# Optimization experiments

Measured on AMD Instinct MI355X. Metric: run time of the kernel, lower is better.

## Reference

```python
import jax, jax.numpy as jnp
import numpy as np

N = 100000   # num nodes
E = 1200000  # num edges (before self-loops)
K = 2        # SGConv propagation hops


def _gcn_norm(edge_index, edge_weight):
    # PyG gcn_norm: add self-loops (weight 1) then symmetric normalization
    loop = jnp.arange(N, dtype=edge_index.dtype)
    src = jnp.concatenate([edge_index[0], loop])
    dst = jnp.concatenate([edge_index[1], loop])
    w = jnp.concatenate([edge_weight, jnp.ones((N,), edge_weight.dtype)])
    deg = jax.ops.segment_sum(w, dst, num_segments=N)
    dinv = jnp.where(deg > 0, jax.lax.rsqrt(deg), jnp.zeros_like(deg))
    norm = dinv[src] * w * dinv[dst]
    return src, dst, norm


def _sgconv(x, src, dst, norm, W, b):
    # K hops of A_hat @ x, then linear: x @ W.T + b
    for _ in range(K):
        x = jax.ops.segment_sum(norm[:, None] * x[src], dst, num_segments=N)
    return x @ W.T + b


def setup_inputs() -> dict:
    key = jax.random.key(0)
    k = jax.random.split(key, 6)
    d_in, d_hid, d_out = 64, 64, 40
    x = jax.random.normal(k[0], (N, d_in), jnp.float32)
    edge_index = jax.random.randint(k[1], (2, E), 0, N, jnp.int32)
    edge_weight = jnp.ones((E,), jnp.float32)
    W1 = jax.random.normal(k[2], (d_hid, d_in), jnp.float32) / np.sqrt(d_in)
    b1 = jnp.zeros((d_hid,), jnp.float32)
    W2 = jax.random.normal(k[3], (d_out, d_hid), jnp.float32) / np.sqrt(d_hid)
    b2 = jnp.zeros((d_out,), jnp.float32)
    return {"x": x, "edge_index": edge_index, "edge_weight": edge_weight,
            "W1": W1, "b1": b1, "W2": W2, "b2": b2}


def reference(x, edge_index, edge_weight, W1, b1, W2, b2):
    # eval mode: F.dropout(p=0.6, training=False) is identity
    src, dst, norm = _gcn_norm(edge_index, edge_weight)
    h = jax.nn.relu(_sgconv(x, src, dst, norm, W1, b1))
    out = _sgconv(h, src, dst, norm, W2, b2)
    return out
```

## Files before the change

kernel.cpp:

```cpp
#include <hip/hip_runtime.h>
#include <hip/hip_fp16.h>


#define SCAN_TPB 256
#define SCAN_ITEMS 8
#define SCAN_CHUNK (SCAN_TPB * SCAN_ITEMS)
#define P1_EDGES 2048
#define MAX_NB 784


__global__ __launch_bounds__(SCAN_TPB) void scan_partial_kernel(const int* __restrict__ cnt,
                                                                int* __restrict__ bsums, int N_) {
    int t = threadIdx.x;
    int base = blockIdx.x * SCAN_CHUNK + t * SCAN_ITEMS;
    int s = 0;
    #pragma unroll
    for (int j = 0; j < SCAN_ITEMS; ++j) { int i = base + j; if (i < N_) s += cnt[i]; }
    __shared__ int sm[SCAN_TPB];
    sm[t] = s; __syncthreads();
    for (int o = SCAN_TPB / 2; o > 0; o >>= 1) {
        if (t < o) sm[t] += sm[t + o];
        __syncthreads();
    }
    if (t == 0) bsums[blockIdx.x] = sm[0];
}

__global__ __launch_bounds__(1024) void scan_bsums_kernel(int* bsums, int nb,
                                                          int* out, int N_) {
    __shared__ int sm[1024];
    int t = threadIdx.x;
    int v = (t < nb) ? bsums[t] : 0;
    sm[t] = v; __syncthreads();
    for (int o = 1; o < 1024; o <<= 1) {
        int u = (t >= o) ? sm[t - o] : 0;
        __syncthreads();
        sm[t] += u;
        __syncthreads();
    }
    if (t < nb) bsums[t] = sm[t] - v;
    if (t == 1023) out[N_] = sm[1023];
}

__global__ __launch_bounds__(SCAN_TPB) void scan_final_kernel(const int* __restrict__ cnt,
                                                              const int* __restrict__ bsums,
                                                              int* __restrict__ out, int N_) {
    int t = threadIdx.x;
    int base = blockIdx.x * SCAN_CHUNK + t * SCAN_ITEMS;
    int loc[SCAN_ITEMS];
    int s = 0;
    #pragma unroll
    for (int j = 0; j < SCAN_ITEMS; ++j) {
        int i = base + j;
        int c = (i < N_) ? cnt[i] : 0;
        loc[j] = s; s += c;
    }
    __shared__ int sm[SCAN_TPB];
    sm[t] = s; __syncthreads();
    for (int o = 1; o < SCAN_TPB; o <<= 1) {
        int u = (t >= o) ? sm[t - o] : 0;
        __syncthreads();
        sm[t] += u;
        __syncthreads();
    }
    int excl = bsums[blockIdx.x] + sm[t] - s;
    #pragma unroll
    for (int j = 0; j < SCAN_ITEMS; ++j) {
        int i = base + j;
        if (i < N_) out[i] = excl + loc[j];
    }
}

__global__ __launch_bounds__(256) void p1_count_kernel(const int* __restrict__ ei,
                                                       int* __restrict__ coarseCnt,
                                                       int E_, int PB, int NB) {
    __shared__ int hist[MAX_NB];
    int tid = threadIdx.x;
    for (int u = tid; u < NB; u += 256) hist[u] = 0;
    __syncthreads();
    int base = blockIdx.x * P1_EDGES;
    #pragma unroll
    for (int j = 0; j < P1_EDGES / 512; ++j) {
        int e = base + j * 512 + tid * 2;
        if (e + 1 < E_) {
            int2 d2 = *(const int2*)&ei[E_ + e];
            atomicAdd(&hist[d2.x >> 7], 1);
            atomicAdd(&hist[d2.y >> 7], 1);
        } else if (e < E_) {
            atomicAdd(&hist[ei[E_ + e] >> 7], 1);
        }
    }
    __syncthreads();
    for (int u = tid; u < NB; u += 256) coarseCnt[u * PB + blockIdx.x] = hist[u];
}

__global__ __launch_bounds__(256) void p1_scatter_kernel(const int* __restrict__ ei,
                                                         const float* __restrict__ w,
                                                         const int* __restrict__ coarseOff,
                                                         int2* __restrict__ sorted,
                                                         int E_, int PB, int NB) {
    __shared__ int lcur[MAX_NB];
    int tid = threadIdx.x;
    for (int u = tid; u < NB; u += 256) lcur[u] = coarseOff[u * PB + blockIdx.x];
    __syncthreads();
    int base = blockIdx.x * P1_EDGES;
    #pragma unroll
    for (int j = 0; j < P1_EDGES / 512; ++j) {
        int e = base + j * 512 + tid * 2;
        if (e + 1 < E_) {
            int2   s2 = *(const int2*)&ei[e];
            int2   d2 = *(const int2*)&ei[E_ + e];
            float2 w2 = *(const float2*)&w[e];
            int p0 = atomicAdd(&lcur[d2.x >> 7], 1);
            sorted[p0] = make_int2(s2.x | ((d2.x & 127) << 17), __float_as_int(w2.x));
            int p1 = atomicAdd(&lcur[d2.y >> 7], 1);
            sorted[p1] = make_int2(s2.y | ((d2.y & 127) << 17), __float_as_int(w2.y));
        } else if (e < E_) {
            int dst = ei[E_ + e];
            int pos = atomicAdd(&lcur[dst >> 7], 1);
            sorted[pos] = make_int2(ei[e] | ((dst & 127) << 17), __float_as_int(w[e]));
        }
    }
}

__global__ __launch_bounds__(256) void p2_fine_kernel(const int2* __restrict__ sorted,
                                                      const int* __restrict__ coarseOff,
                                                      int2* __restrict__ edge,
                                                      int* __restrict__ row_ptr,
                                                      float* __restrict__ dinv,
                                                      int N_, int E_, int PB, int NB) {
    __shared__ int fcnt[128], fexc[128], fcur[128];
    __shared__ float fdeg[128];
    const int b = blockIdx.x;
    const int tid = threadIdx.x;
    const int start = coarseOff[b * PB];
    const int end = (b + 1 < NB) ? coarseOff[(b + 1) * PB] : E_;
    if (tid < 128) { fcnt[tid] = 0; fdeg[tid] = 1.0f; }
    __syncthreads();
    for (int p = start + tid; p < end; p += 256)
        atomicAdd(&fcnt[sorted[p].x >> 17], 1);
    __syncthreads();
    if (tid < 128) fexc[tid] = fcnt[tid];
    __syncthreads();
    for (int o = 1; o < 128; o <<= 1) {
        int v = (tid < 128 && tid >= o) ? fexc[tid - o] : 0;
        __syncthreads();
        if (tid < 128) fexc[tid] += v;
        __syncthreads();
    }
    const int node0 = b << 7;
    if (tid < 128) {
        fexc[tid] -= fcnt[tid];
        fcur[tid] = 0;
        int node = node0 + tid;
        if (node < N_) row_ptr[node] = start + fexc[tid];
    }
    __syncthreads();
    for (int p = start + tid; p < end; p += 256) {
        int2 pk = sorted[p];
        int fine = pk.x >> 17;
        int src  = pk.x & 0x1FFFF;
        int r = atomicAdd(&fcur[fine], 1);
        atomicAdd(&fdeg[fine], __int_as_float(pk.y));
        edge[start + fexc[fine] + r] = make_int2(src, pk.y);
    }
    __syncthreads();
    if (tid < 128) {
        int node = node0 + tid;
        if (node < N_) {
            float s = fdeg[tid];
            dinv[node] = (s > 0.f) ? (1.0f / sqrtf(s)) : 0.f;
        }
    }
    if (b == 0 && tid == 0) row_ptr[N_] = E_;
}

#define FMA_MIX_LO(accv, hbits, vw) \
    asm("v_fma_mix_f32 %0, %1, %2, %0 op_sel_hi:[1,0,0]" : "+v"(accv) : "v"(hbits), "v"(vw))
#define FMA_MIX_HI(accv, hbits, vw) \
    asm("v_fma_mix_f32 %0, %1, %2, %0 op_sel:[1,0,0] op_sel_hi:[1,0,0]" : "+v"(accv) : "v"(hbits), "v"(vw))

template<int NL, int EPI>
__global__ __launch_bounds__(256) void hop_h_kernel(const __half* __restrict__ xin,
                                                    void* __restrict__ xout,
                                                    const float* __restrict__ dinv,
                                                    const int* __restrict__ row_ptr,
                                                    const int2* __restrict__ edge,
                                                    const float* __restrict__ bias, int N_) {
    int wave = (blockIdx.x * blockDim.x + threadIdx.x) >> 6;
    int lane = threadIdx.x & 63;
    const int g   = lane >> 4;
    const int hl  = lane & 15;
    const int hle = (NL == 16) ? hl : min(hl, NL - 1);

    int nd = wave * 4 + g;
    bool real = nd < N_;
    int d = real ? nd : (N_ - 1);

    int e0 = row_ptr[d];
    int nE = real ? (row_ptr[d + 1] - e0) : 0;
    float di = dinv[d];
    float2 selfv = ((const float2*)(xin + (size_t)d * 64))[hle];
    float acc[4] = {0.f, 0.f, 0.f, 0.f};

    int maxNE = nE;
    maxNE = max(maxNE, __shfl_xor(maxNE, 16));
    maxNE = max(maxNE, __shfl_xor(maxNE, 32));

    for (int eb = 0; eb < maxNE; eb += 16) {
        int rem = nE - eb;
        int2 ev = (hl < rem) ? edge[e0 + eb + hl] : make_int2(d, 0);
        int mm = min(16, maxNE - eb);
        for (int j = 0; j < mm; j += 2) {
            int   s0 = __shfl(ev.x, (g << 4) | j);
            int   s1 = __shfl(ev.x, (g << 4) | (j + 1));
            float v0 = __shfl(__int_as_float(ev.y), (g << 4) | j);
            float v1 = __shfl(__int_as_float(ev.y), (g << 4) | (j + 1));
            float2 x0 = ((const float2*)(xin + (size_t)s0 * 64))[hle];
            float2 x1 = ((const float2*)(xin + (size_t)s1 * 64))[hle];
            FMA_MIX_LO(acc[0], x0.x, v0); FMA_MIX_HI(acc[1], x0.x, v0);
            FMA_MIX_LO(acc[2], x0.y, v0); FMA_MIX_HI(acc[3], x0.y, v0);
            FMA_MIX_LO(acc[0], x1.x, v1); FMA_MIX_HI(acc[1], x1.x, v1);
            FMA_MIX_LO(acc[2], x1.y, v1); FMA_MIX_HI(acc[3], x1.y, v1);
        }
    }
    const float one = 1.0f;
    FMA_MIX_LO(acc[0], selfv.x, one); FMA_MIX_HI(acc[1], selfv.x, one);
    FMA_MIX_LO(acc[2], selfv.y, one); FMA_MIX_HI(acc[3], selfv.y, one);

    float sc = (EPI == 0) ? di * di : di;
    #pragma unroll
    for (int u = 0; u < 4; ++u) acc[u] *= sc;

    if (real && hl < NL) {
        if constexpr (EPI == 0) {
            float2 pk;
            ((__half2*)&pk)[0] = __floats2half2_rn(acc[0], acc[1]);
            ((__half2*)&pk)[1] = __floats2half2_rn(acc[2], acc[3]);
            ((float2*)((__half*)xout + (size_t)d * 64))[hl] = pk;
        } else if constexpr (EPI == 1) {
            float4 bv = ((const float4*)bias)[hl];
            float2 pk;
            ((__half2*)&pk)[0] = __floats2half2_rn(fmaxf(acc[0] + bv.x, 0.f),
                                                   fmaxf(acc[1] + bv.y, 0.f));
            ((__half2*)&pk)[1] = __floats2half2_rn(fmaxf(acc[2] + bv.z, 0.f),
                                                   fmaxf(acc[3] + bv.w, 0.f));
            ((float2*)((__half*)xout + (size_t)d * 64))[hl] = pk;
        } else {
            float4 bv = ((const float4*)bias)[hl];
            float4 r = make_float4(acc[0] + bv.x, acc[1] + bv.y,
                                   acc[2] + bv.z, acc[3] + bv.w);
            *(float4*)((float*)xout + (size_t)d * 40 + hl * 4) = r;
        }
    }
}

template<int F, bool INH>
__global__ __launch_bounds__(256, 4) void linear_tiled_kernel(const void* __restrict__ hin,
                                                              __half* __restrict__ outp,
                                                              const float* __restrict__ W,
                                                              const float* __restrict__ dinv,
                                                              int N_) {
    constexpr int BM = 64;
    __shared__ float hs[BM * 64];
    __shared__ float ws[64 * 64];
    const int tid  = threadIdx.x;
    const int base = blockIdx.x * BM;

    for (int u = tid; u < 64 * 16; u += 256) {
        int f = u >> 4, kc = u & 15;
        float4 v = (f < F) ? ((const float4*)W)[f * 16 + kc]
                           : make_float4(0.f, 0.f, 0.f, 0.f);
        *(float4*)&ws[f * 64 + ((kc ^ ((f >> 2) & 7)) << 2)] = v;
    }
    const int lim = min(BM, N_ - base);
    for (int u = tid; u < BM * 16; u += 256) {
        int n = u >> 4, kc = u & 15;
        float4 v;
        if (n < lim) {
            if constexpr (INH) {
                float2 hv = ((const float2*)((const __half*)hin + (size_t)(base + n) * 64))[kc];
                const __half2* hh = (const __half2*)&hv;
                float2 a = __half22float2(hh[0]);
                float2 b = __half22float2(hh[1]);
                v = make_float4(a.x, a.y, b.x, b.y);
            } else {
                v = ((const float4*)((const float*)hin + (size_t)(base + n) * 64))[kc];
            }
        } else v = make_float4(0.f, 0.f, 0.f, 0.f);
        *(float4*)&hs[n * 64 + ((kc ^ ((n >> 2) & 7)) << 2)] = v;
    }
    __syncthreads();

    const int f0 = (tid & 15) << 2;
    const int n0 = (tid >> 4) << 2;
    float4 acc[4];
    #pragma unroll
    for (int i = 0; i < 4; ++i) acc[i] = make_float4(0.f, 0.f, 0.f, 0.f);

    #pragma unroll 2
    for (int kc = 0; kc < 16; ++kc) {
        float4 hv[4], wv[4];
        #pragma unroll
        for (int i = 0; i < 4; ++i) {
            int n = n0 + i;
            hv[i] = *(const float4*)&hs[n * 64 + ((kc ^ ((n >> 2) & 7)) << 2)];
        }
        #pragma unroll
        for (int j = 0; j < 4; ++j) {
            int f = f0 + j;
            wv[j] = *(const float4*)&ws[f * 64 + ((kc ^ ((f >> 2) & 7)) << 2)];
        }
        #pragma unroll
        for (int i = 0; i < 4; ++i) {
            acc[i].x = fmaf(hv[i].x, wv[0].x, acc[i].x);
            acc[i].x = fmaf(hv[i].y, wv[0].y, acc[i].x);
            acc[i].x = fmaf(hv[i].z, wv[0].z, acc[i].x);
            acc[i].x = fmaf(hv[i].w, wv[0].w, acc[i].x);
            acc[i].y = fmaf(hv[i].x, wv[1].x, acc[i].y);
            acc[i].y = fmaf(hv[i].y, wv[1].y, acc[i].y);
            acc[i].y = fmaf(hv[i].z, wv[1].z, acc[i].y);
            acc[i].y = fmaf(hv[i].w, wv[1].w, acc[i].y);
            acc[i].z = fmaf(hv[i].x, wv[2].x, acc[i].z);
            acc[i].z = fmaf(hv[i].y, wv[2].y, acc[i].z);
            acc[i].z = fmaf(hv[i].z, wv[2].z, acc[i].z);
            acc[i].z = fmaf(hv[i].w, wv[2].w, acc[i].z);
            acc[i].w = fmaf(hv[i].x, wv[3].x, acc[i].w);
            acc[i].w = fmaf(hv[i].y, wv[3].y, acc[i].w);
            acc[i].w = fmaf(hv[i].z, wv[3].z, acc[i].w);
            acc[i].w = fmaf(hv[i].w, wv[3].w, acc[i].w);
        }
    }

    if (f0 < F) {
        #pragma unroll
        for (int i = 0; i < 4; ++i) {
            int n = base + n0 + i;
            if (n < N_) {
                float dn = dinv[n];
                __half* o = outp + (size_t)n * 64 + f0;
                ((__half2*)o)[0] = __floats2half2_rn(acc[i].x * dn, acc[i].y * dn);
                ((__half2*)o)[1] = __floats2half2_rn(acc[i].z * dn, acc[i].w * dn);
            }
        }
    }
}

extern "C" void kernel_launch(void* const* d_in, const int* in_sizes, int n_in,
                              void* d_out, int out_size, void* d_ws, size_t ws_size,
                              hipStream_t stream) {
    const float* x   = (const float*)d_in[0];
    const int*   ei  = (const int*)d_in[1];
    const float* w   = (const float*)d_in[2];
    const float* W1  = (const float*)d_in[3];
    const float* b1  = (const float*)d_in[4];
    const float* W2  = (const float*)d_in[5];
    const float* b2  = (const float*)d_in[6];
    float* out = (float*)d_out;

    const int N_ = in_sizes[0] / 64;
    const int E_ = in_sizes[2];
    const int PB = (E_ + P1_EDGES - 1) / P1_EDGES;
    const int NB = (N_ + 127) >> 7;
    const int M  = NB * PB;

    char* ws = (char*)d_ws;
    size_t off = 0;
    auto alloc = [&](size_t bytes) { size_t o = off; off += (bytes + 255) & ~(size_t)255; return o; };
    float* dinv      = (float*)(ws + alloc((size_t)N_ * 4));
    int*   row_ptr   = (int*)  (ws + alloc(((size_t)N_ + 1) * 4));
    int*   bsums     = (int*)  (ws + alloc(1024 * 4));
    int*   coarseCnt = (int*)  (ws + alloc((size_t)M * 4));
    int*   coarseOff = (int*)  (ws + alloc(((size_t)M + 1) * 4));
    int2*  edge      = (int2*) (ws + alloc((size_t)E_ * 8));
    float* bufA      = (float*)(ws + alloc((size_t)N_ * 64 * 4));
    float* bufB      = (float*)(ws + alloc((size_t)N_ * 64 * 4));
    int2*   sorted = (int2*)bufA;
    __half* hA0    = (__half*)bufA;
    __half* hLo    = (__half*)bufB;
    __half* hHi    = (__half*)((char*)bufB + (size_t)N_ * 64 * 2);
    (void)ws_size; (void)n_in; (void)out_size;

    const int bh4 = (N_ + 15) / 16;
    const int nbs = (M + SCAN_CHUNK - 1) / SCAN_CHUNK;
    const int bl_ = (N_ + 63) / 64;

    p1_count_kernel<<<PB, 256, 0, stream>>>(ei, coarseCnt, E_, PB, NB);
    scan_partial_kernel<<<nbs, SCAN_TPB, 0, stream>>>(coarseCnt, bsums, M);
    scan_bsums_kernel<<<1, 1024, 0, stream>>>(bsums, nbs, coarseOff, M);
    scan_final_kernel<<<nbs, SCAN_TPB, 0, stream>>>(coarseCnt, bsums, coarseOff, M);
    p1_scatter_kernel<<<PB, 256, 0, stream>>>(ei, w, coarseOff, sorted, E_, PB, NB);
    p2_fine_kernel<<<NB, 256, 0, stream>>>(sorted, coarseOff, edge, row_ptr, dinv, N_, E_, PB, NB);

    linear_tiled_kernel<64, false><<<bl_, 256, 0, stream>>>(x, hLo, W1, dinv, N_);
    hop_h_kernel<16, 0><<<bh4, 256, 0, stream>>>(hLo, hHi, dinv, row_ptr, edge, nullptr, N_);
    hop_h_kernel<16, 1><<<bh4, 256, 0, stream>>>(hHi, hA0, dinv, row_ptr, edge, b1, N_);
    linear_tiled_kernel<40, true><<<bl_, 256, 0, stream>>>(hA0, hLo, W2, dinv, N_);
    hop_h_kernel<10, 0><<<bh4, 256, 0, stream>>>(hLo, hHi, dinv, row_ptr, edge, nullptr, N_);
    hop_h_kernel<10, 2><<<bh4, 256, 0, stream>>>(hHi, out, dinv, row_ptr, edge, b2, N_);
}
```

Measured before the change: 207.9 us.

## Widen coarse sort buckets to 256 nodes and prefetch edges in hop kernel

The two-level counting sort now buckets destinations by 256 nodes instead of 128. This halves the coarse histogram size and the number of fine-sort blocks, and lets all 256 threads of the fine kernel take part in its scan and writes. The hop kernel software-prefetches the next 16-edge chunk and unrolls the gather loop by four, so more independent row loads are in flight. The wider unroll assumes neighbour counts padded to multiples of four; padding lanes read the node's own row with weight 0. That is extra traffic but stays correct.

```diff
diff --git a/kernel.cpp b/kernel.cpp
--- a/kernel.cpp
+++ b/kernel.cpp
@@ -6,7 +6,7 @@
 #define SCAN_ITEMS 8
 #define SCAN_CHUNK (SCAN_TPB * SCAN_ITEMS)
 #define P1_EDGES 2048
-#define MAX_NB 784
+#define MAX_NB 392
 
 
 __global__ __launch_bounds__(SCAN_TPB) void scan_partial_kernel(const int* __restrict__ cnt,
@@ -83,10 +83,10 @@
         int e = base + j * 512 + tid * 2;
         if (e + 1 < E_) {
             int2 d2 = *(const int2*)&ei[E_ + e];
-            atomicAdd(&hist[d2.x >> 7], 1);
-            atomicAdd(&hist[d2.y >> 7], 1);
+            atomicAdd(&hist[d2.x >> 8], 1);
+            atomicAdd(&hist[d2.y >> 8], 1);
         } else if (e < E_) {
-            atomicAdd(&hist[ei[E_ + e] >> 7], 1);
+            atomicAdd(&hist[ei[E_ + e] >> 8], 1);
         }
     }
     __syncthreads();
@@ -110,14 +110,14 @@
             int2   s2 = *(const int2*)&ei[e];
             int2   d2 = *(const int2*)&ei[E_ + e];
             float2 w2 = *(const float2*)&w[e];
-            int p0 = atomicAdd(&lcur[d2.x >> 7], 1);
-            sorted[p0] = make_int2(s2.x | ((d2.x & 127) << 17), __float_as_int(w2.x));
-            int p1 = atomicAdd(&lcur[d2.y >> 7], 1);
-            sorted[p1] = make_int2(s2.y | ((d2.y & 127) << 17), __float_as_int(w2.y));
+            int p0 = atomicAdd(&lcur[d2.x >> 8], 1);
+            sorted[p0] = make_int2(s2.x | ((d2.x & 255) << 17), __float_as_int(w2.x));
+            int p1 = atomicAdd(&lcur[d2.y >> 8], 1);
+            sorted[p1] = make_int2(s2.y | ((d2.y & 255) << 17), __float_as_int(w2.y));
         } else if (e < E_) {
             int dst = ei[E_ + e];
-            int pos = atomicAdd(&lcur[dst >> 7], 1);
-            sorted[pos] = make_int2(ei[e] | ((dst & 127) << 17), __float_as_int(w[e]));
+            int pos = atomicAdd(&lcur[dst >> 8], 1);
+            sorted[pos] = make_int2(ei[e] | ((dst & 255) << 17), __float_as_int(w[e]));
         }
     }
 }
@@ -128,48 +128,43 @@
                                                       int* __restrict__ row_ptr,
                                                       float* __restrict__ dinv,
                                                       int N_, int E_, int PB, int NB) {
-    __shared__ int fcnt[128], fexc[128], fcur[128];
-    __shared__ float fdeg[128];
+    __shared__ int fcnt[256], fexc[256], fcur[256];
+    __shared__ float fdeg[256];
     const int b = blockIdx.x;
     const int tid = threadIdx.x;
     const int start = coarseOff[b * PB];
     const int end = (b + 1 < NB) ? coarseOff[(b + 1) * PB] : E_;
-    if (tid < 128) { fcnt[tid] = 0; fdeg[tid] = 1.0f; }
+    fcnt[tid] = 0; fdeg[tid] = 1.0f;
     __syncthreads();
     for (int p = start + tid; p < end; p += 256)
-        atomicAdd(&fcnt[sorted[p].x >> 17], 1);
-    __syncthreads();
-    if (tid < 128) fexc[tid] = fcnt[tid];
-    __syncthreads();
-    for (int o = 1; o < 128; o <<= 1) {
-        int v = (tid < 128 && tid >= o) ? fexc[tid - o] : 0;
-        __syncthreads();
-        if (tid < 128) fexc[tid] += v;
-        __syncthreads();
-    }
-    const int node0 = b << 7;
-    if (tid < 128) {
-        fexc[tid] -= fcnt[tid];
-        fcur[tid] = 0;
-        int node = node0 + tid;
-        if (node < N_) row_ptr[node] = start + fexc[tid];
-    }
+        atomicAdd(&fcnt[(sorted[p].x >> 17) & 255], 1);
+    __syncthreads();
+    fexc[tid] = fcnt[tid];
+    __syncthreads();
+    for (int o = 1; o < 256; o <<= 1) {
+        int v = (tid >= o) ? fexc[tid - o] : 0;
+        __syncthreads();
+        fexc[tid] += v;
+        __syncthreads();
+    }
+    const int node0 = b << 8;
+    fexc[tid] -= fcnt[tid];
+    fcur[tid] = 0;
+    int node = node0 + tid;
+    if (node < N_) row_ptr[node] = start + fexc[tid];
     __syncthreads();
     for (int p = start + tid; p < end; p += 256) {
         int2 pk = sorted[p];
-        int fine = pk.x >> 17;
+        int fine = (pk.x >> 17) & 255;
         int src  = pk.x & 0x1FFFF;
         int r = atomicAdd(&fcur[fine], 1);
         atomicAdd(&fdeg[fine], __int_as_float(pk.y));
         edge[start + fexc[fine] + r] = make_int2(src, pk.y);
     }
     __syncthreads();
-    if (tid < 128) {
-        int node = node0 + tid;
-        if (node < N_) {
-            float s = fdeg[tid];
-            dinv[node] = (s > 0.f) ? (1.0f / sqrtf(s)) : 0.f;
-        }
+    if (node < N_) {
+        float s = fdeg[tid];
+        dinv[node] = (s > 0.f) ? (1.0f / sqrtf(s)) : 0.f;
     }
     if (b == 0 && tid == 0) row_ptr[N_] = E_;
 }
@@ -206,22 +201,35 @@
     maxNE = max(maxNE, __shfl_xor(maxNE, 16));
     maxNE = max(maxNE, __shfl_xor(maxNE, 32));
 
+    const int2 pad = make_int2(d, 0);
+    int2 ev = (hl < nE) ? edge[e0 + hl] : pad;
     for (int eb = 0; eb < maxNE; eb += 16) {
-        int rem = nE - eb;
-        int2 ev = (hl < rem) ? edge[e0 + eb + hl] : make_int2(d, 0);
+        int nxt = eb + 16;
+        int2 evn = (nxt < maxNE && hl < nE - nxt) ? edge[e0 + nxt + hl] : pad;
         int mm = min(16, maxNE - eb);
-        for (int j = 0; j < mm; j += 2) {
+        for (int j = 0; j < mm; j += 4) {
             int   s0 = __shfl(ev.x, (g << 4) | j);
             int   s1 = __shfl(ev.x, (g << 4) | (j + 1));
+            int   s2 = __shfl(ev.x, (g << 4) | (j + 2));
+            int   s3 = __shfl(ev.x, (g << 4) | (j + 3));
             float v0 = __shfl(__int_as_float(ev.y), (g << 4) | j);
             float v1 = __shfl(__int_as_float(ev.y), (g << 4) | (j + 1));
+            float v2 = __shfl(__int_as_float(ev.y), (g << 4) | (j + 2));
+            float v3 = __shfl(__int_as_float(ev.y), (g << 4) | (j + 3));
             float2 x0 = ((const float2*)(xin + (size_t)s0 * 64))[hle];
             float2 x1 = ((const float2*)(xin + (size_t)s1 * 64))[hle];
+            float2 x2 = ((const float2*)(xin + (size_t)s2 * 64))[hle];
+            float2 x3 = ((const float2*)(xin + (size_t)s3 * 64))[hle];
             FMA_MIX_LO(acc[0], x0.x, v0); FMA_MIX_HI(acc[1], x0.x, v0);
             FMA_MIX_LO(acc[2], x0.y, v0); FMA_MIX_HI(acc[3], x0.y, v0);
             FMA_MIX_LO(acc[0], x1.x, v1); FMA_MIX_HI(acc[1], x1.x, v1);
             FMA_MIX_LO(acc[2], x1.y, v1); FMA_MIX_HI(acc[3], x1.y, v1);
-        }
+            FMA_MIX_LO(acc[0], x2.x, v2); FMA_MIX_HI(acc[1], x2.x, v2);
+            FMA_MIX_LO(acc[2], x2.y, v2); FMA_MIX_HI(acc[3], x2.y, v2);
+            FMA_MIX_LO(acc[0], x3.x, v3); FMA_MIX_HI(acc[1], x3.x, v3);
+            FMA_MIX_LO(acc[2], x3.y, v3); FMA_MIX_HI(acc[3], x3.y, v3);
+        }
+        ev = evn;
     }
     const float one = 1.0f;
     FMA_MIX_LO(acc[0], selfv.x, one); FMA_MIX_HI(acc[1], selfv.x, one);
@@ -360,7 +368,7 @@
     const int N_ = in_sizes[0] / 64;
     const int E_ = in_sizes[2];
     const int PB = (E_ + P1_EDGES - 1) / P1_EDGES;
-    const int NB = (N_ + 127) >> 7;
+    const int NB = (N_ + 255) >> 8;
     const int M  = NB * PB;
 
     char* ws = (char*)d_ws;
```

After: 198.2 us. -4.6%, faster.
